# Kernel tuning notes

Measured on AMD Instinct MI355X. Metric: run time of the kernel, lower is better.

## Reference

```python
import jax, jax.numpy as jnp
import numpy as np

VOCAB = 50000
B, S = 256, 512
M1, M2, EMB = 1024, 512, 256


def setup_inputs() -> dict:
    key = jax.random.key(0)
    k_idx, k1, k2, k3, kb1, kb2, kb3 = jax.random.split(key, 7)
    idx = jax.random.randint(k_idx, (B, S), 0, VOCAB)
    # torch Linear weights are [out, in]
    W1 = jax.random.normal(k1, (M1, VOCAB), dtype=jnp.float32) * (1.0 / np.sqrt(VOCAB))
    b1 = jax.random.normal(kb1, (M1,), dtype=jnp.float32) * 0.01
    W2 = jax.random.normal(k2, (M2, M1), dtype=jnp.float32) * (1.0 / np.sqrt(M1))
    b2 = jax.random.normal(kb2, (M2,), dtype=jnp.float32) * 0.01
    W3 = jax.random.normal(k3, (EMB, M2), dtype=jnp.float32) * (1.0 / np.sqrt(M2))
    b3 = jax.random.normal(kb3, (EMB,), dtype=jnp.float32) * 0.01
    return {"idx": idx, "W1": W1, "b1": b1, "W2": W2, "b2": b2, "W3": W3, "b3": b3}


def make_bow_vector(idx, vocab_size):
    # vectorized scatter-add histogram: vec[i, idx[i, j]] += 1
    batch = idx.shape[0]
    rows = jnp.arange(batch)[:, None]  # [B, 1] broadcast against [B, S]
    return jnp.zeros((batch, vocab_size), dtype=jnp.float32).at[rows, idx].add(1.0)


def reference(idx, W1, b1, W2, b2, W3, b3):
    bow = make_bow_vector(idx, W1.shape[1])            # [B, V]
    h = jax.nn.relu(bow @ W1.T + b1)                   # [B, M1]
    h = jax.nn.relu(h @ W2.T + b2)                     # [B, M2]
    emb = jax.nn.relu(h @ W3.T + b3)                   # [B, EMB]
    return emb
```

## Files before the change

### kernel.cpp

```cpp
#include <hip/hip_runtime.h>
#include <hip/hip_bf16.h>

#define VOCAB   50000
#define BATCH   256
#define SEQ     512
#define NM1     1024
#define NM2     512
#define NEMB    256
#define KB1     782
#define KPAD    (KB1*64)
#define SPLITK  32

typedef __attribute__((ext_vector_type(8))) short short8;
typedef __attribute__((ext_vector_type(4))) float f32x4;

#define BOW_BYTES   ((size_t)BATCH * KPAD * 4)
#define PART_BYTES  ((size_t)SPLITK * BATCH * NM1 * 4)

__device__ __forceinline__ short f2b(float x) {
    __hip_bfloat16 b = __float2bfloat16(x);
    return __builtin_bit_cast(short, b);
}

__global__ void BOW_hist(const int* __restrict__ idx, float* __restrict__ bow) {
    int i = blockIdx.x;
    int t = threadIdx.x;
    #pragma unroll
    for (int j = t; j < SEQ; j += 256) {
        int v = idx[i * SEQ + j];
        atomicAdd(&bow[(size_t)i * KPAD + v], 1.0f);
    }
}

__global__ __launch_bounds__(512) void BOW_gemm1(
        const float* __restrict__ bow,
        const float* __restrict__ W1,
        float* __restrict__ partials)
{
    __shared__ __align__(16) __hip_bfloat16 As[256 * 64];
    __shared__ __align__(16) __hip_bfloat16 Bs[128 * 64];

    const int tid = threadIdx.x;
    const int bid = blockIdx.x;
    const int s   = bid >> 3;
    const int nt  = bid & 7;
    const int n0  = nt * 128;

    const int kb_start = s * 24 + (s < 14 ? s : 14);
    const int kb_count = 24 + (s < 14 ? 1 : 0);

    const int lane = tid & 63;
    const int w    = tid >> 6;
    const int wm   = w >> 1;
    const int wn   = w & 1;

    f32x4 acc[4][4];
    #pragma unroll
    for (int m = 0; m < 4; m++)
        #pragma unroll
        for (int n = 0; n < 4; n++) acc[m][n] = (f32x4){0.f, 0.f, 0.f, 0.f};

    for (int kb = kb_start; kb < kb_start + kb_count; ++kb) {
        const int kg0 = kb * 64;

        #pragma unroll
        for (int r = 0; r < 4; r++) {
            int c   = tid + 512 * r;
            int row = c >> 3;
            int k8  = c & 7;
            const float* src = bow + (size_t)row * KPAD + kg0 + k8 * 8;
            float4 v0 = *reinterpret_cast<const float4*>(src);
            float4 v1 = *reinterpret_cast<const float4*>(src + 4);
            short8 p;
            p[0] = f2b(v0.x); p[1] = f2b(v0.y); p[2] = f2b(v0.z); p[3] = f2b(v0.w);
            p[4] = f2b(v1.x); p[5] = f2b(v1.y); p[6] = f2b(v1.z); p[7] = f2b(v1.w);
            int dst = row * 64 + ((k8 * 8) ^ ((row & 7) << 3));
            *reinterpret_cast<short8*>(&As[dst]) = p;
        }
        #pragma unroll
        for (int r = 0; r < 2; r++) {
            int c   = tid + 512 * r;
            int row = c >> 3;
            int k8  = c & 7;
            int kg  = kg0 + k8 * 8;
            float4 v0 = {0.f,0.f,0.f,0.f}, v1 = {0.f,0.f,0.f,0.f};
            if (kg < VOCAB) {
                const float* src = W1 + (size_t)(n0 + row) * VOCAB + kg;
                v0 = *reinterpret_cast<const float4*>(src);
                v1 = *reinterpret_cast<const float4*>(src + 4);
            }
            short8 p;
            p[0] = f2b(v0.x); p[1] = f2b(v0.y); p[2] = f2b(v0.z); p[3] = f2b(v0.w);
            p[4] = f2b(v1.x); p[5] = f2b(v1.y); p[6] = f2b(v1.z); p[7] = f2b(v1.w);
            int dst = row * 64 + ((k8 * 8) ^ ((row & 7) << 3));
            *reinterpret_cast<short8*>(&Bs[dst]) = p;
        }
        __syncthreads();

        #pragma unroll
        for (int kk = 0; kk < 2; kk++) {
            short8 a[4], b[4];
            const int kf = kk * 32 + ((lane >> 4) << 3);
            #pragma unroll
            for (int m = 0; m < 4; m++) {
                int row = wm * 64 + m * 16 + (lane & 15);
                int e   = row * 64 + (kf ^ ((row & 7) << 3));
                a[m] = *reinterpret_cast<const short8*>(&As[e]);
            }
            #pragma unroll
            for (int n = 0; n < 4; n++) {
                int row = wn * 64 + n * 16 + (lane & 15);
                int e   = row * 64 + (kf ^ ((row & 7) << 3));
                b[n] = *reinterpret_cast<const short8*>(&Bs[e]);
            }
            #pragma unroll
            for (int m = 0; m < 4; m++)
                #pragma unroll
                for (int n = 0; n < 4; n++)
                    acc[m][n] = __builtin_amdgcn_mfma_f32_16x16x32_bf16(
                                    a[m], b[n], acc[m][n], 0, 0, 0);
        }
        __syncthreads();
    }

    float* dst = partials + (size_t)s * (BATCH * NM1);
    #pragma unroll
    for (int m = 0; m < 4; m++) {
        #pragma unroll
        for (int n = 0; n < 4; n++) {
            int col = n0 + wn * 64 + n * 16 + (lane & 15);
            #pragma unroll
            for (int j = 0; j < 4; j++) {
                int rowi = wm * 64 + m * 16 + ((lane >> 4) * 4 + j);
                dst[(size_t)rowi * NM1 + col] = acc[m][n][j];
            }
        }
    }
}

__global__ void BOW_reduce1(const float* __restrict__ partials,
                            const float* __restrict__ b1,
                            float* __restrict__ h1) {
    int o = blockIdx.x * 256 + threadIdx.x;
    int m = o & (NM1 - 1);
    float s = b1[m];
    #pragma unroll
    for (int sp = 0; sp < SPLITK; sp++) s += partials[(size_t)sp * (BATCH * NM1) + o];
    h1[o] = fmaxf(s, 0.f);
}

__global__ void BOW_gemm_f32(const float* __restrict__ A,
                             const float* __restrict__ Bw,
                             const float* __restrict__ bias,
                             float* __restrict__ out,
                             int N, int K) {
    __shared__ float As[32][33];
    __shared__ float Bs[32][33];
    int tid = threadIdx.x;
    int i0 = blockIdx.y * 32, n0 = blockIdx.x * 32;
    int r = tid >> 5, c = tid & 31;
    int ty = tid >> 4, tx = tid & 15;
    float a2[2][2] = {{0.f, 0.f}, {0.f, 0.f}};

    for (int k0 = 0; k0 < K; k0 += 32) {
        #pragma unroll
        for (int rr = 0; rr < 4; rr++) {
            As[r + rr * 8][c] = A[(size_t)(i0 + r + rr * 8) * K + k0 + c];
            Bs[r + rr * 8][c] = Bw[(size_t)(n0 + r + rr * 8) * K + k0 + c];
        }
        __syncthreads();
        #pragma unroll
        for (int k = 0; k < 32; k++) {
            float av0 = As[ty * 2][k],     av1 = As[ty * 2 + 1][k];
            float bv0 = Bs[tx * 2][k],     bv1 = Bs[tx * 2 + 1][k];
            a2[0][0] += av0 * bv0; a2[0][1] += av0 * bv1;
            a2[1][0] += av1 * bv0; a2[1][1] += av1 * bv1;
        }
        __syncthreads();
    }
    #pragma unroll
    for (int ii = 0; ii < 2; ii++)
        #pragma unroll
        for (int nn = 0; nn < 2; nn++) {
            int i = i0 + ty * 2 + ii, n = n0 + tx * 2 + nn;
            out[(size_t)i * N + n] = fmaxf(a2[ii][nn] + bias[n], 0.f);
        }
}

extern "C" void kernel_launch(void* const* d_in, const int* in_sizes, int n_in,
                              void* d_out, int out_size, void* d_ws, size_t ws_size,
                              hipStream_t stream) {
    const int*   idx = (const int*)d_in[0];
    const float* W1  = (const float*)d_in[1];
    const float* b1  = (const float*)d_in[2];
    const float* W2  = (const float*)d_in[3];
    const float* b2  = (const float*)d_in[4];
    const float* W3  = (const float*)d_in[5];
    const float* b3  = (const float*)d_in[6];
    float* out = (float*)d_out;

    char* ws = (char*)d_ws;
    float* bow      = (float*)ws;
    float* partials = (float*)(ws + BOW_BYTES);
    float* h1       = (float*)(ws + BOW_BYTES + PART_BYTES);
    float* h2       = h1 + BATCH * NM1;

    hipMemsetAsync(bow, 0, BOW_BYTES, stream);
    BOW_hist<<<BATCH, 256, 0, stream>>>(idx, bow);
    BOW_gemm1<<<SPLITK * 8, 512, 0, stream>>>(bow, W1, partials);
    BOW_reduce1<<<(BATCH * NM1) / 256, 256, 0, stream>>>(partials, b1, h1);
    BOW_gemm_f32<<<dim3(NM2 / 32, BATCH / 32), 256, 0, stream>>>(h1, W2, b2, h2, NM2, NM1);
    BOW_gemm_f32<<<dim3(NEMB / 32, BATCH / 32), 256, 0, stream>>>(h2, W3, b3, out, NEMB, NM2);
}
```

Before: 433.2 us.

## Build bf16 BOW histogram in LDS and DMA it directly into GEMM tiles

The histogram is now built in shared memory with packed 16-bit counters per half-row and written out as bf16. This replaces the memset plus float global atomics and halves the BOW buffer size. The GEMM loads the A tile straight into LDS with global_load_lds, applying the swizzle on the source side, and narrows the N tile to 64 so the grid has twice as many blocks. The trade-off is that each block re-reads the A tile twice as often and does less MFMA work per tile.

New measurement: 405.5 us. 6.4% less time.

```diff
diff --git a/kernel.cpp b/kernel.cpp
--- a/kernel.cpp
+++ b/kernel.cpp
@@ -10,41 +10,66 @@
 #define KB1     782
 #define KPAD    (KB1*64)
 #define SPLITK  32
+#define NT      16
+#define HHALF   (KPAD/2)
 
 typedef __attribute__((ext_vector_type(8))) short short8;
 typedef __attribute__((ext_vector_type(4))) float f32x4;
 
-#define BOW_BYTES   ((size_t)BATCH * KPAD * 4)
+#define BOW_BYTES   ((size_t)BATCH * KPAD * 2)
 #define PART_BYTES  ((size_t)SPLITK * BATCH * NM1 * 4)
 
 __device__ __forceinline__ short f2b(float x) {
     __hip_bfloat16 b = __float2bfloat16(x);
     return __builtin_bit_cast(short, b);
 }
-
-__global__ void BOW_hist(const int* __restrict__ idx, float* __restrict__ bow) {
-    int i = blockIdx.x;
-    int t = threadIdx.x;
-    #pragma unroll
-    for (int j = t; j < SEQ; j += 256) {
-        int v = idx[i * SEQ + j];
-        atomicAdd(&bow[(size_t)i * KPAD + v], 1.0f);
+__device__ __forceinline__ unsigned short f2bu(float x) {
+    __hip_bfloat16 b = __float2bfloat16(x);
+    return __builtin_bit_cast(unsigned short, b);
+}
+
+__global__ __launch_bounds__(256) void BOW_hist2(const int* __restrict__ idx,
+                                                 __hip_bfloat16* __restrict__ bow) {
+    __shared__ unsigned int h[HHALF / 2];
+    const int b    = blockIdx.x;
+    const int row  = b >> 1;
+    const int lo   = (b & 1) * HHALF;
+    const int t    = threadIdx.x;
+
+    for (int j = t; j < HHALF / 2; j += 256) h[j] = 0u;
+    __syncthreads();
+
+    #pragma unroll
+    for (int u = 0; u < 2; u++) {
+        int v = idx[row * SEQ + u * 256 + t];
+        int d = v - lo;
+        if ((unsigned)d < (unsigned)HHALF)
+            atomicAdd(&h[d >> 1], (d & 1) ? 0x10000u : 1u);
+    }
+    __syncthreads();
+
+    unsigned int* dst = (unsigned int*)(bow + (size_t)row * KPAD + lo);
+    for (int j = t; j < HHALF / 2; j += 256) {
+        unsigned int w  = h[j];
+        unsigned int l16 = f2bu((float)(w & 0xFFFFu));
+        unsigned int h16 = f2bu((float)(w >> 16));
+        dst[j] = l16 | (h16 << 16);
     }
 }
 
 __global__ __launch_bounds__(512) void BOW_gemm1(
-        const float* __restrict__ bow,
+        const __hip_bfloat16* __restrict__ bow,
         const float* __restrict__ W1,
         float* __restrict__ partials)
 {
     __shared__ __align__(16) __hip_bfloat16 As[256 * 64];
-    __shared__ __align__(16) __hip_bfloat16 Bs[128 * 64];
+    __shared__ __align__(16) __hip_bfloat16 Bs[64 * 64];
 
     const int tid = threadIdx.x;
     const int bid = blockIdx.x;
-    const int s   = bid >> 3;
-    const int nt  = bid & 7;
-    const int n0  = nt * 128;
+    const int s   = bid >> 4;
+    const int nt  = bid & 15;
+    const int n0  = nt * 64;
 
     const int kb_start = s * 24 + (s < 14 ? s : 14);
     const int kb_count = 24 + (s < 14 ? 1 : 0);
@@ -54,52 +79,50 @@
     const int wm   = w >> 1;
     const int wn   = w & 1;
 
-    f32x4 acc[4][4];
+    f32x4 acc[4][2];
     #pragma unroll
     for (int m = 0; m < 4; m++)
         #pragma unroll
-        for (int n = 0; n < 4; n++) acc[m][n] = (f32x4){0.f, 0.f, 0.f, 0.f};
+        for (int n = 0; n < 2; n++) acc[m][n] = (f32x4){0.f, 0.f, 0.f, 0.f};
+
+    const int brow = tid >> 3;
+    const int bk8  = tid & 7;
+    const int bdst = brow * 64 + ((bk8 * 8) ^ ((brow & 7) << 3));
+    const float* wsrc = W1 + (size_t)(n0 + brow) * VOCAB + bk8 * 8;
 
     for (int kb = kb_start; kb < kb_start + kb_count; ++kb) {
         const int kg0 = kb * 64;
 
         #pragma unroll
-        for (int r = 0; r < 4; r++) {
-            int c   = tid + 512 * r;
+        for (int i = 0; i < 4; i++) {
+            int c   = i * 512 + tid;
             int row = c >> 3;
             int k8  = c & 7;
-            const float* src = bow + (size_t)row * KPAD + kg0 + k8 * 8;
-            float4 v0 = *reinterpret_cast<const float4*>(src);
-            float4 v1 = *reinterpret_cast<const float4*>(src + 4);
+            const __hip_bfloat16* src =
+                bow + (size_t)row * KPAD + kg0 + ((k8 * 8) ^ ((row & 7) << 3));
+            __builtin_amdgcn_global_load_lds(
+                (const __attribute__((address_space(1))) void*)src,
+                (__attribute__((address_space(3))) void*)&As[c * 8], 16, 0, 0);
+        }
+
+        {
+            int kg = kg0 + bk8 * 8;
+            float4 v0 = {0.f,0.f,0.f,0.f}, v1 = {0.f,0.f,0.f,0.f};
+            if (kg < VOCAB) {
+                const float* src = wsrc + kg0;
+                v0 = *reinterpret_cast<const float4*>(src);
+                v1 = *reinterpret_cast<const float4*>(src + 4);
+            }
             short8 p;
             p[0] = f2b(v0.x); p[1] = f2b(v0.y); p[2] = f2b(v0.z); p[3] = f2b(v0.w);
             p[4] = f2b(v1.x); p[5] = f2b(v1.y); p[6] = f2b(v1.z); p[7] = f2b(v1.w);
-            int dst = row * 64 + ((k8 * 8) ^ ((row & 7) << 3));
-            *reinterpret_cast<short8*>(&As[dst]) = p;
-        }
-        #pragma unroll
-        for (int r = 0; r < 2; r++) {
-            int c   = tid + 512 * r;
-            int row = c >> 3;
-            int k8  = c & 7;
-            int kg  = kg0 + k8 * 8;
-            float4 v0 = {0.f,0.f,0.f,0.f}, v1 = {0.f,0.f,0.f,0.f};
-            if (kg < VOCAB) {
-                const float* src = W1 + (size_t)(n0 + row) * VOCAB + kg;
-                v0 = *reinterpret_cast<const float4*>(src);
-                v1 = *reinterpret_cast<const float4*>(src + 4);
-            }
-            short8 p;
-            p[0] = f2b(v0.x); p[1] = f2b(v0.y); p[2] = f2b(v0.z); p[3] = f2b(v0.w);
-            p[4] = f2b(v1.x); p[5] = f2b(v1.y); p[6] = f2b(v1.z); p[7] = f2b(v1.w);
-            int dst = row * 64 + ((k8 * 8) ^ ((row & 7) << 3));
-            *reinterpret_cast<short8*>(&Bs[dst]) = p;
+            *reinterpret_cast<short8*>(&Bs[bdst]) = p;
         }
         __syncthreads();
 
         #pragma unroll
         for (int kk = 0; kk < 2; kk++) {
-            short8 a[4], b[4];
+            short8 a[4], b[2];
             const int kf = kk * 32 + ((lane >> 4) << 3);
             #pragma unroll
             for (int m = 0; m < 4; m++) {
@@ -108,15 +131,15 @@
                 a[m] = *reinterpret_cast<const short8*>(&As[e]);
             }
             #pragma unroll
-            for (int n = 0; n < 4; n++) {
-                int row = wn * 64 + n * 16 + (lane & 15);
+            for (int n = 0; n < 2; n++) {
+                int row = wn * 32 + n * 16 + (lane & 15);
                 int e   = row * 64 + (kf ^ ((row & 7) << 3));
                 b[n] = *reinterpret_cast<const short8*>(&Bs[e]);
             }
             #pragma unroll
             for (int m = 0; m < 4; m++)
                 #pragma unroll
-                for (int n = 0; n < 4; n++)
+                for (int n = 0; n < 2; n++)
                     acc[m][n] = __builtin_amdgcn_mfma_f32_16x16x32_bf16(
                                     a[m], b[n], acc[m][n], 0, 0, 0);
         }
@@ -127,8 +150,8 @@
     #pragma unroll
     for (int m = 0; m < 4; m++) {
         #pragma unroll
-        for (int n = 0; n < 4; n++) {
-            int col = n0 + wn * 64 + n * 16 + (lane & 15);
+        for (int n = 0; n < 2; n++) {
+            int col = n0 + wn * 32 + n * 16 + (lane & 15);
             #pragma unroll
             for (int j = 0; j < 4; j++) {
                 int rowi = wm * 64 + m * 16 + ((lane >> 4) * 4 + j);
@@ -200,14 +223,13 @@
     float* out = (float*)d_out;
 
     char* ws = (char*)d_ws;
-    float* bow      = (float*)ws;
+    __hip_bfloat16* bow = (__hip_bfloat16*)ws;
     float* partials = (float*)(ws + BOW_BYTES);
     float* h1       = (float*)(ws + BOW_BYTES + PART_BYTES);
     float* h2       = h1 + BATCH * NM1;
 
-    hipMemsetAsync(bow, 0, BOW_BYTES, stream);
-    BOW_hist<<<BATCH, 256, 0, stream>>>(idx, bow);
-    BOW_gemm1<<<SPLITK * 8, 512, 0, stream>>>(bow, W1, partials);
+    BOW_hist2<<<BATCH * 2, 256, 0, stream>>>(idx, bow);
+    BOW_gemm1<<<SPLITK * NT, 512, 0, stream>>>(bow, W1, partials);
     BOW_reduce1<<<(BATCH * NM1) / 256, 256, 0, stream>>>(partials, b1, h1);
     BOW_gemm_f32<<<dim3(NM2 / 32, BATCH / 32), 256, 0, stream>>>(h1, W2, b2, h2, NM2, NM1);
     BOW_gemm_f32<<<dim3(NEMB / 32, BATCH / 32), 256, 0, stream>>>(h2, W3, b3, out, NEMB, NM2);
```
